# Kernel optimization log

Hardware: AMD Instinct MI355X
Metric: run time of the kernel (lower is better)

The kernel has to match this reference:

```python
import jax, jax.numpy as jnp
import numpy as np

B, N = 8, 6                 # batch, cameras
D, C = 45, 64               # depth bins, context channels
FH, FW = 8, 22              # feature-map height/width
GX, GY, GZ = 64, 64, 32     # BEV grid: W, H, D in the torch code
RES = 0.5
XOFF, YOFF, ZOFF = 16.0, 16.0, 8.0


def _frustum():
    # matches LSS.create_frustum: pixel coords over full 352x128 image, depths 1..45
    xs = jnp.linspace(0.0, 351.0, FW)
    ys = jnp.linspace(0.0, 127.0, FH)
    ds = jnp.arange(1.0, 46.0, 1.0)
    d, y, x = jnp.meshgrid(ds, ys, xs, indexing='ij')   # [D, FH, FW]
    return jnp.stack([x * d, y * d, d], axis=-1)         # [D, FH, FW, 3]


def setup_inputs() -> dict:
    key = jax.random.key(0)
    k1, k2, k3 = jax.random.split(key, 3)
    # depthNet output: softmax over depth bins
    depth = jax.nn.softmax(jax.random.normal(k1, (B, N, D, FH, FW), dtype=jnp.float32), axis=2)
    feature = jax.random.normal(k2, (B, N, C, FH, FW), dtype=jnp.float32)
    # realistic pinhole intrinsics (invertible), identity rotations, small translations
    K = jnp.array([[250.0, 0.0, 176.0], [0.0, 250.0, 64.0], [0.0, 0.0, 1.0]], dtype=jnp.float32)
    intrinsics = jnp.tile(K, (B, N, 1, 1))
    rots = jnp.tile(jnp.eye(3, dtype=jnp.float32), (B, N, 1, 1))
    trans = jax.random.normal(k3, (B, N, 3), dtype=jnp.float32) * 0.5
    return {"depth": depth, "feature": feature, "rots": rots, "trans": trans, "intrinsics": intrinsics}


def reference(depth, feature, rots, trans, intrinsics):
    fr = _frustum()                                              # [D, FH, FW, 3]
    # get_geometry: unproject frustum to world
    inv_K = jnp.linalg.inv(intrinsics)                           # [B, N, 3, 3]
    pts_c = jnp.einsum('bnij,dhwj->bndhwi', inv_K, fr)           # camera frame
    geom = jnp.einsum('bnij,bndhwj->bndhwi', rots, pts_c) + trans[:, :, None, None, None, :]

    # context = depth outer-product feature: [B, N, D, C, FH, FW] -> [B,N,D,FH,FW,C]
    ctx = (depth[:, :, :, None] * feature[:, :, None]).transpose(0, 1, 2, 4, 5, 3)
    ctx = ctx.reshape(-1, C)                                     # [P, C]
    g = geom.reshape(-1, 3)                                      # [P, 3]

    # voxel index compute (astype int truncates toward zero, matching torch .long())
    nx = ((g[:, 0] + XOFF) / RES).astype(jnp.int32)
    ny = ((g[:, 2] + YOFF) / RES).astype(jnp.int32)
    nz = ((g[:, 1] + ZOFF) / RES).astype(jnp.int32)
    valid = (nx >= 0) & (nx < GX) & (ny >= 0) & (ny < GY) & (nz >= 0) & (nz < GZ)

    bidx = jnp.repeat(jnp.arange(B, dtype=jnp.int32), N * D * FH * FW)
    idx = jnp.where(valid, bidx * (GX * GY * GZ) + nx * (GY * GZ) + ny * GZ + nz, 0)

    # scatter-sum into dense BEV grid; invalid points contribute zero
    bev = jnp.zeros((B * GX * GY * GZ, C), dtype=ctx.dtype)
    bev = bev.at[idx].add(ctx * valid[:, None].astype(ctx.dtype))
    # [B, GX, GY, GZ, C] -> [B, C, GZ, GX, GY]
    return bev.reshape(B, GX, GY, GZ, C).transpose(0, 4, 3, 1, 2)
```

## Files before the change

### kernel.cpp

```cpp
#include <hip/hip_runtime.h>

#define BB 8
#define NN 6
#define DD 45
#define CC 64
#define FHH 8
#define FWW 22
#define GXX 64
#define GYY 64
#define GZZ 32
#define NPOINTS (BB*NN*DD*FHH*FWW)
#define NSITES (BB*NN*FHH*FWW)
#define NFEATT (NSITES*CC)
#define ROWS (BB*GZZ)
#define CAPR 8192

#define WS_CNT_OFF 0
#define WS_BUCKET_OFF 1024
#define WS_FEATT_OFF (WS_BUCKET_OFF + (size_t)ROWS * CAPR * 8)
#define WS_NEEDED (WS_FEATT_OFF + (size_t)NFEATT * 4)

__global__ __launch_bounds__(256) void lss_zero(float4* __restrict__ p, int n4) {
    int i = blockIdx.x * blockDim.x + threadIdx.x;
    int stride = gridDim.x * blockDim.x;
    float4 z = make_float4(0.f, 0.f, 0.f, 0.f);
    for (; i < n4; i += stride) p[i] = z;
}

__global__ __launch_bounds__(256) void lss_featT(const float* __restrict__ feature,
                                                 float* __restrict__ featT,
                                                 int* __restrict__ cnt) {
    int idx = blockIdx.x * 256 + threadIdx.x;
    if (idx < ROWS) cnt[idx] = 0;
    int c = idx & 63;
    int site = idx >> 6;
    int hw = site % (FHH * FWW);
    int cam = site / (FHH * FWW);
    featT[idx] = feature[(cam * CC + c) * (FHH * FWW) + hw];
}

__global__ __launch_bounds__(256) void lss_build(
    const float* __restrict__ depth,
    const float* __restrict__ rots, const float* __restrict__ trans,
    const float* __restrict__ intr,
    int* __restrict__ cnt, int2* __restrict__ bucket2)
{
    int p = blockIdx.x * 256 + threadIdx.x;
    int lane = threadIdx.x & 63;
    int w = p % FWW;
    int t = p / FWW;
    int h = t % FHH; t /= FHH;
    int di = t % DD; t /= DD;
    int n = t % NN;
    int b = t / NN;

    float d = (float)(di + 1);
    float x = (float)(351.0 * (double)w / 21.0);
    float y = (float)(127.0 * (double)h / 7.0);

    const float* K = intr + (b * NN + n) * 9;
    double k00 = K[0], k01 = K[1], k02 = K[2];
    double k10 = K[3], k11 = K[4], k12 = K[5];
    double k20 = K[6], k21 = K[7], k22 = K[8];
    double det = k00 * (k11 * k22 - k12 * k21)
               - k01 * (k10 * k22 - k12 * k20)
               + k02 * (k10 * k21 - k11 * k20);
    double id = 1.0 / det;
    float i00 = (float)(( k11 * k22 - k12 * k21) * id);
    float i01 = (float)((-k01 * k22 + k02 * k21) * id);
    float i02 = (float)(( k01 * k12 - k02 * k11) * id);
    float i10 = (float)((-k10 * k22 + k12 * k20) * id);
    float i11 = (float)(( k00 * k22 - k02 * k20) * id);
    float i12 = (float)((-k00 * k12 + k02 * k10) * id);
    float i20 = (float)(( k10 * k21 - k11 * k20) * id);
    float i21 = (float)((-k00 * k21 + k01 * k20) * id);
    float i22 = (float)(( k00 * k11 - k01 * k10) * id);

    float p0 = x * d, p1 = y * d, p2 = d;
    float c0 = i00 * p0 + i01 * p1 + i02 * p2;
    float c1 = i10 * p0 + i11 * p1 + i12 * p2;
    float c2 = i20 * p0 + i21 * p1 + i22 * p2;

    const float* R = rots + (b * NN + n) * 9;
    const float* T = trans + (b * NN + n) * 3;
    float g0 = R[0] * c0 + R[1] * c1 + R[2] * c2 + T[0];
    float g1 = R[3] * c0 + R[4] * c1 + R[5] * c2 + T[1];
    float g2 = R[6] * c0 + R[7] * c1 + R[8] * c2 + T[2];

    int nx = (int)((g0 + 16.0f) / 0.5f);
    int ny = (int)((g2 + 16.0f) / 0.5f);
    int nz = (int)((g1 + 8.0f)  / 0.5f);
    bool valid = (nx >= 0) & (nx < GXX) & (ny >= 0) & (ny < GYY) & (nz >= 0) & (nz < GZZ);

    int row = valid ? (b * GZZ + nz) : -1;
    int site = (((b * NN + n) * FHH) + h) * FWW + w;
    int meta = (site << 12) | (nx << 6) | ny;
    float dv = depth[p];

    unsigned long long active = __ballot(valid);
    while (active) {
        int leader = __ffsll((unsigned long long)active) - 1;
        int lrow = __shfl(row, leader);
        unsigned long long same = __ballot(valid && (row == lrow));
        int base = 0;
        if (lane == leader) base = atomicAdd(&cnt[lrow], (int)__popcll(same));
        base = __shfl(base, leader);
        if (valid && (row == lrow)) {
            int off = (int)__popcll(same & ((1ull << lane) - 1ull));
            int rank = base + off;
            if (rank < CAPR) bucket2[lrow * CAPR + rank] = make_int2(__float_as_int(dv), meta);
        }
        active &= ~same;
    }
}

__global__ __launch_bounds__(256) void lss_out4(
    const float* __restrict__ featT,
    const int* __restrict__ cnt, const int2* __restrict__ bucket2,
    float* __restrict__ out)
{
    int bid = blockIdx.x;
    int ccb = bid & 15;
    int row = bid >> 4;
    int b = row >> 5;
    int nz = row & 31;
    int tid = threadIdx.x;

    int scnt = cnt[row];
    if (scnt > CAPR) scnt = CAPR;

    size_t ob0 = (((size_t)b * CC + ccb * 4) * GZZ + nz) * (GXX * GYY);
    const size_t cstride = (size_t)GZZ * GXX * GYY;

    if (scnt == 0) {
        float4 z = make_float4(0.f, 0.f, 0.f, 0.f);
        #pragma unroll
        for (int cc = 0; cc < 4; ++cc) {
            size_t ob = ob0 + (size_t)cc * cstride;
            for (int i = tid; i < 1024; i += 256)
                *(float4*)(out + ob + i * 4) = z;
        }
        return;
    }

    __shared__ float acc[4][GXX * GYY];
    {
        float4 z = make_float4(0.f, 0.f, 0.f, 0.f);
        float4* a4 = (float4*)acc;
        for (int i = tid; i < 4 * GXX * GYY / 4; i += 256) a4[i] = z;
    }
    __syncthreads();

    const float4* fT = (const float4*)featT;
    const int2* bk = bucket2 + (size_t)row * CAPR;
    for (int e = tid; e < scnt; e += 256) {
        int2 en = bk[e];
        float dv = __int_as_float(en.x);
        int meta = en.y;
        int site = meta >> 12;
        int nxny = meta & 4095;
        float4 f = fT[site * 16 + ccb];
        atomicAdd(&acc[0][nxny], dv * f.x);
        atomicAdd(&acc[1][nxny], dv * f.y);
        atomicAdd(&acc[2][nxny], dv * f.z);
        atomicAdd(&acc[3][nxny], dv * f.w);
    }
    __syncthreads();

    #pragma unroll
    for (int cc = 0; cc < 4; ++cc) {
        const float4* a4 = (const float4*)acc[cc];
        size_t ob = ob0 + (size_t)cc * cstride;
        for (int i = tid; i < 1024; i += 256)
            *(float4*)(out + ob + i * 4) = a4[i];
    }
}

__global__ __launch_bounds__(256) void lss_scatter_direct(
    const float* __restrict__ depth, const float* __restrict__ feature,
    const float* __restrict__ rots, const float* __restrict__ trans,
    const float* __restrict__ intr, float* __restrict__ out)
{
    int p = blockIdx.x * 4 + (threadIdx.x >> 6);
    int lane = threadIdx.x & 63;
    int w = p % FWW;
    int t = p / FWW;
    int h = t % FHH; t /= FHH;
    int di = t % DD; t /= DD;
    int n = t % NN;
    int b = t / NN;
    float d = (float)(di + 1);
    float x = (float)(351.0 * (double)w / 21.0);
    float y = (float)(127.0 * (double)h / 7.0);
    const float* K = intr + (b * NN + n) * 9;
    double k00 = K[0], k01 = K[1], k02 = K[2];
    double k10 = K[3], k11 = K[4], k12 = K[5];
    double k20 = K[6], k21 = K[7], k22 = K[8];
    double det = k00*(k11*k22-k12*k21) - k01*(k10*k22-k12*k20) + k02*(k10*k21-k11*k20);
    double id = 1.0 / det;
    float i00=(float)((k11*k22-k12*k21)*id), i01=(float)((-k01*k22+k02*k21)*id), i02=(float)((k01*k12-k02*k11)*id);
    float i10=(float)((-k10*k22+k12*k20)*id), i11=(float)((k00*k22-k02*k20)*id), i12=(float)((-k00*k12+k02*k10)*id);
    float i20=(float)((k10*k21-k11*k20)*id), i21=(float)((-k00*k21+k01*k20)*id), i22=(float)((k00*k11-k01*k10)*id);
    float p0 = x * d, p1 = y * d, p2 = d;
    float c0 = i00*p0 + i01*p1 + i02*p2;
    float c1 = i10*p0 + i11*p1 + i12*p2;
    float c2 = i20*p0 + i21*p1 + i22*p2;
    const float* R = rots + (b * NN + n) * 9;
    const float* T = trans + (b * NN + n) * 3;
    float g0 = R[0]*c0 + R[1]*c1 + R[2]*c2 + T[0];
    float g1 = R[3]*c0 + R[4]*c1 + R[5]*c2 + T[1];
    float g2 = R[6]*c0 + R[7]*c1 + R[8]*c2 + T[2];
    int nx = (int)((g0 + 16.0f) / 0.5f);
    int ny = (int)((g2 + 16.0f) / 0.5f);
    int nz = (int)((g1 + 8.0f)  / 0.5f);
    if (!((nx >= 0) & (nx < GXX) & (ny >= 0) & (ny < GYY) & (nz >= 0) & (nz < GZZ)))
        return;
    float dv = depth[(((b * NN + n) * DD + di) * FHH + h) * FWW + w];
    float fv = feature[(((b * NN + n) * CC + lane) * FHH + h) * FWW + w];
    size_t oidx = ((((size_t)b * CC + lane) * GZZ + nz) * GXX + nx) * GYY + ny;
    atomicAdd(out + oidx, dv * fv);
}

extern "C" void kernel_launch(void* const* d_in, const int* in_sizes, int n_in,
                              void* d_out, int out_size, void* d_ws, size_t ws_size,
                              hipStream_t stream) {
    const float* depth   = (const float*)d_in[0];
    const float* feature = (const float*)d_in[1];
    const float* rots    = (const float*)d_in[2];
    const float* trans   = (const float*)d_in[3];
    const float* intr    = (const float*)d_in[4];
    float* out = (float*)d_out;

    if (ws_size >= WS_NEEDED) {
        int*   cnt     = (int*)((char*)d_ws + WS_CNT_OFF);
        int2*  bucket2 = (int2*)((char*)d_ws + WS_BUCKET_OFF);
        float* featT   = (float*)((char*)d_ws + WS_FEATT_OFF);

        lss_featT<<<NFEATT / 256, 256, 0, stream>>>(feature, featT, cnt);
        lss_build<<<NPOINTS / 256, 256, 0, stream>>>(depth, rots, trans, intr, cnt, bucket2);
        lss_out4<<<ROWS * 16, 256, 0, stream>>>(featT, cnt, bucket2, out);
    } else {
        lss_zero<<<4096, 256, 0, stream>>>((float4*)out, out_size / 4);
        lss_scatter_direct<<<NPOINTS / 4, 256, 0, stream>>>(depth, feature, rots, trans, intr, out);
    }
}
```

Before: 97.37 us.

## Split output kernel to one channel per block with channel-major features and nontemporal stores

The output kernel now assigns one (batch, channel, z) plane per block instead of four channels per block. This raises the block count fourfold and cuts shared memory from 64KB to 16KB, which allows higher occupancy. The output plane is contiguous, so it is written with nontemporal vector stores. Feature data is laid out channel-major so each block reads a contiguous slice. The cost is that every bucket entry is now read four times as often, once per channel block instead of once per four channels.

```diff
diff --git a/kernel.cpp b/kernel.cpp
--- a/kernel.cpp
+++ b/kernel.cpp
@@ -15,10 +15,12 @@
 #define ROWS (BB*GZZ)
 #define CAPR 8192
 
+typedef float f32x4 __attribute__((ext_vector_type(4)));
+
 #define WS_CNT_OFF 0
 #define WS_BUCKET_OFF 1024
-#define WS_FEATT_OFF (WS_BUCKET_OFF + (size_t)ROWS * CAPR * 8)
-#define WS_NEEDED (WS_FEATT_OFF + (size_t)NFEATT * 4)
+#define WS_FEATC_OFF (WS_BUCKET_OFF + (size_t)ROWS * CAPR * 8)
+#define WS_NEEDED (WS_FEATC_OFF + (size_t)NFEATT * 4)
 
 __global__ __launch_bounds__(256) void lss_zero(float4* __restrict__ p, int n4) {
     int i = blockIdx.x * blockDim.x + threadIdx.x;
@@ -27,16 +29,16 @@
     for (; i < n4; i += stride) p[i] = z;
 }
 
-__global__ __launch_bounds__(256) void lss_featT(const float* __restrict__ feature,
-                                                 float* __restrict__ featT,
+__global__ __launch_bounds__(256) void lss_featC(const float* __restrict__ feature,
+                                                 float* __restrict__ featC,
                                                  int* __restrict__ cnt) {
     int idx = blockIdx.x * 256 + threadIdx.x;
     if (idx < ROWS) cnt[idx] = 0;
-    int c = idx & 63;
-    int site = idx >> 6;
+    int site = idx % NSITES;
+    int c = idx / NSITES;
     int hw = site % (FHH * FWW);
     int cam = site / (FHH * FWW);
-    featT[idx] = feature[(cam * CC + c) * (FHH * FWW) + hw];
+    featC[idx] = feature[(cam * CC + c) * (FHH * FWW) + hw];
 }
 
 __global__ __launch_bounds__(256) void lss_build(
@@ -114,44 +116,41 @@
     }
 }
 
-__global__ __launch_bounds__(256) void lss_out4(
-    const float* __restrict__ featT,
+__global__ __launch_bounds__(256) void lss_out5(
+    const float* __restrict__ featC,
     const int* __restrict__ cnt, const int2* __restrict__ bucket2,
     float* __restrict__ out)
 {
     int bid = blockIdx.x;
-    int ccb = bid & 15;
-    int row = bid >> 4;
-    int b = row >> 5;
-    int nz = row & 31;
+    int nz = bid & 31;
+    int c  = (bid >> 5) & 63;
+    int b  = bid >> 11;
+    int row = (b << 5) | nz;
     int tid = threadIdx.x;
 
     int scnt = cnt[row];
     if (scnt > CAPR) scnt = CAPR;
 
-    size_t ob0 = (((size_t)b * CC + ccb * 4) * GZZ + nz) * (GXX * GYY);
-    const size_t cstride = (size_t)GZZ * GXX * GYY;
+    f32x4* oplane = (f32x4*)(out + (size_t)bid * (GXX * GYY));
 
     if (scnt == 0) {
-        float4 z = make_float4(0.f, 0.f, 0.f, 0.f);
+        f32x4 z = (f32x4){0.f, 0.f, 0.f, 0.f};
         #pragma unroll
-        for (int cc = 0; cc < 4; ++cc) {
-            size_t ob = ob0 + (size_t)cc * cstride;
-            for (int i = tid; i < 1024; i += 256)
-                *(float4*)(out + ob + i * 4) = z;
-        }
+        for (int k = 0; k < 4; ++k)
+            __builtin_nontemporal_store(z, oplane + tid + k * 256);
         return;
     }
 
-    __shared__ float acc[4][GXX * GYY];
+    __shared__ float acc[GXX * GYY];
+    f32x4* a4 = (f32x4*)acc;
     {
-        float4 z = make_float4(0.f, 0.f, 0.f, 0.f);
-        float4* a4 = (float4*)acc;
-        for (int i = tid; i < 4 * GXX * GYY / 4; i += 256) a4[i] = z;
+        f32x4 z = (f32x4){0.f, 0.f, 0.f, 0.f};
+        #pragma unroll
+        for (int k = 0; k < 4; ++k) a4[tid + k * 256] = z;
     }
     __syncthreads();
 
-    const float4* fT = (const float4*)featT;
+    const float* fslice = featC + (size_t)c * NSITES;
     const int2* bk = bucket2 + (size_t)row * CAPR;
     for (int e = tid; e < scnt; e += 256) {
         int2 en = bk[e];
@@ -159,21 +158,13 @@
         int meta = en.y;
         int site = meta >> 12;
         int nxny = meta & 4095;
-        float4 f = fT[site * 16 + ccb];
-        atomicAdd(&acc[0][nxny], dv * f.x);
-        atomicAdd(&acc[1][nxny], dv * f.y);
-        atomicAdd(&acc[2][nxny], dv * f.z);
-        atomicAdd(&acc[3][nxny], dv * f.w);
+        atomicAdd(&acc[nxny], dv * fslice[site]);
     }
     __syncthreads();
 
     #pragma unroll
-    for (int cc = 0; cc < 4; ++cc) {
-        const float4* a4 = (const float4*)acc[cc];
-        size_t ob = ob0 + (size_t)cc * cstride;
-        for (int i = tid; i < 1024; i += 256)
-            *(float4*)(out + ob + i * 4) = a4[i];
-    }
+    for (int k = 0; k < 4; ++k)
+        __builtin_nontemporal_store(a4[tid + k * 256], oplane + tid + k * 256);
 }
 
 __global__ __launch_bounds__(256) void lss_scatter_direct(
@@ -234,11 +225,11 @@
     if (ws_size >= WS_NEEDED) {
         int*   cnt     = (int*)((char*)d_ws + WS_CNT_OFF);
         int2*  bucket2 = (int2*)((char*)d_ws + WS_BUCKET_OFF);
-        float* featT   = (float*)((char*)d_ws + WS_FEATT_OFF);
-
-        lss_featT<<<NFEATT / 256, 256, 0, stream>>>(feature, featT, cnt);
+        float* featC   = (float*)((char*)d_ws + WS_FEATC_OFF);
+
+        lss_featC<<<NFEATT / 256, 256, 0, stream>>>(feature, featC, cnt);
         lss_build<<<NPOINTS / 256, 256, 0, stream>>>(depth, rots, trans, intr, cnt, bucket2);
-        lss_out4<<<ROWS * 16, 256, 0, stream>>>(featT, cnt, bucket2, out);
+        lss_out5<<<BB * CC * GZZ, 256, 0, stream>>>(featC, cnt, bucket2, out);
     } else {
         lss_zero<<<4096, 256, 0, stream>>>((float4*)out, out_size / 4);
         lss_scatter_direct<<<NPOINTS / 4, 256, 0, stream>>>(depth, feature, rots, trans, intr, out);
```

Result: slower. 244.6 us (+151.2%).
